# Kernel optimization log

Hardware: AMD Instinct MI355X
Metric: run time of the kernel (lower is better)

The kernel has to match this reference:

```python
import jax, jax.numpy as jnp
import numpy as np

B, R, C, A, K = 32, 13, 13, 5, 20
CELL = K + 5                      # 4 coords + objectness + 20 classes
N = R * C * A                     # 845 boxes per image
THRESH = 0.5
NMS_TH = 0.4
BIAS_VALS = [1.3221, 1.73145, 3.19275, 4.00944, 5.05587,
             8.09892, 9.47112, 4.84053, 11.2364, 10.0071]


def setup_inputs() -> dict:
    key = jax.random.key(0)
    x = jax.random.normal(key, (B, R, C, A * CELL), dtype=jnp.float32)
    bias = jnp.array(BIAS_VALS, dtype=jnp.float32)  # anchor priors (w,h interleaved)
    return {"x": x, "bias": bias}


def _nms_keep(iou, scores):
    """Greedy per-class NMS. iou: [B,N,N]; scores: [B,K,N] (already thresholded).
    Returns bool keep mask [B,K,N]. Decisions are non-differentiable, so inputs
    are stop_gradient'ed by the caller."""
    Bn = scores.shape[0]
    valid = scores > THRESH
    order = jnp.argsort(-scores, axis=-1)          # descending score order [B,K,N]
    rank = jnp.argsort(order, axis=-1)             # inverse permutation   [B,K,N]
    barange = jnp.arange(Bn)[:, None]

    def body(i, suppressed):
        idx = order[:, :, i]                                              # [B,K]
        sup_i = jnp.take_along_axis(suppressed, idx[:, :, None], -1)[..., 0]
        val_i = jnp.take_along_axis(valid, idx[:, :, None], -1)[..., 0]
        alive = val_i & ~sup_i                                            # [B,K]
        row = iou[barange, idx]                                           # [B,K,N]
        return suppressed | (alive[..., None] & (row > NMS_TH) & (rank > i))

    suppressed = jax.lax.fori_loop(0, N, body, jnp.zeros((Bn, K, N), bool))
    return valid & ~suppressed


def reference(x, bias):
    Bn, R_, C_, _ = x.shape
    t = x.reshape(Bn, R_, C_, A, CELL)
    gx = jnp.arange(C_, dtype=x.dtype)
    gy = jnp.arange(R_, dtype=x.dtype)
    # box decode (matches source: hNorm=rows used for width, wNorm=cols for height)
    bx = (jax.nn.sigmoid(t[..., 0]) + gx[None, None, :, None]) / C_
    by = (jax.nn.sigmoid(t[..., 1]) + gy[None, :, None, None]) / R_
    bw = jnp.exp(t[..., 2]) * bias[0::2] / R_
    bh = jnp.exp(t[..., 3]) * bias[1::2] / C_
    obj = jax.nn.sigmoid(t[..., 4])
    cls = jax.nn.softmax(t[..., 5:], axis=-1)
    prob = obj[..., None] * cls
    prob = jnp.where(prob > THRESH, prob, 0.0)

    # flatten to box index layout (y*cols + x)*anchors + a, same as source
    flat = lambda a: a.reshape(Bn, N)
    bx, by, bw, bh, obj = map(flat, (bx, by, bw, bh, obj))
    prob = prob.reshape(Bn, N, K)

    # corner-form boxes for IoU (source uses x - w/2, y - h/2, w, h)
    x1 = bx - bw * 0.5
    y1 = by - bh * 0.5
    x2 = x1 + bw
    y2 = y1 + bh
    iw = jnp.maximum(0.0, jnp.minimum(x2[:, :, None], x2[:, None, :]) -
                          jnp.maximum(x1[:, :, None], x1[:, None, :]))
    ih = jnp.maximum(0.0, jnp.minimum(y2[:, :, None], y2[:, None, :]) -
                          jnp.maximum(y1[:, :, None], y1[:, None, :]))
    inter = iw * ih
    area = bw * bh
    union = area[:, :, None] + area[:, None, :] - inter
    iou = inter / jnp.maximum(union, 1e-9)                       # [B,N,N]

    scores = prob.transpose(0, 2, 1)                             # [B,K,N]
    keep = _nms_keep(jax.lax.stop_gradient(iou),
                     jax.lax.stop_gradient(scores))
    out_prob = jnp.where(keep, scores, 0.0).transpose(0, 2, 1)   # [B,N,K]

    out = jnp.concatenate([bx[..., None], by[..., None], bw[..., None],
                           bh[..., None], obj[..., None], out_prob], axis=-1)
    return out  # [B, N, CELL]
```

## Files before the change

kernel.cpp:

```cpp
#include <hip/hip_runtime.h>
#include <math.h>

#define BN 32
#define RR 13
#define CC 13
#define AA 5
#define KK 20
#define CELLSZ 25
#define NN (RR * CC * AA)
#define NBK (BN * KK)
#define THRESH 0.5f
#define NMS_TH 0.4f

#define CAND_OFF 4096
#define REC 8
#define CAP NN

__device__ __forceinline__ float sigmoidf_(float x) {
    return 1.0f / (1.0f + expf(-x));
}

__global__ __launch_bounds__(256) void decode_kernel(
        const float* __restrict__ x,
        const float* __restrict__ bias,
        float* __restrict__ out,
        int* __restrict__ cnt,
        float* __restrict__ cand) {
    int idx = blockIdx.x * 256 + threadIdx.x;
    if (idx >= BN * NN) return;
    int b   = idx / NN;
    int n   = idx % NN;
    int r   = n / (CC * AA);
    int rem = n % (CC * AA);
    int c   = rem / AA;
    int a   = rem % AA;

    const float* t = x + (size_t)idx * CELLSZ;

    float bx  = (sigmoidf_(t[0]) + (float)c) / (float)CC;
    float by  = (sigmoidf_(t[1]) + (float)r) / (float)RR;
    float bw  = expf(t[2]) * bias[2 * a]     / (float)RR;
    float bh  = expf(t[3]) * bias[2 * a + 1] / (float)CC;
    float obj = sigmoidf_(t[4]);

    float l[KK];
    float m = t[5];
#pragma unroll
    for (int k = 0; k < KK; ++k) { l[k] = t[5 + k]; m = fmaxf(m, l[k]); }
    float s = 0.0f;
#pragma unroll
    for (int k = 0; k < KK; ++k) { l[k] = expf(l[k] - m); s += l[k]; }

    float* o = out + (size_t)idx * CELLSZ;
    o[0] = bx; o[1] = by; o[2] = bw; o[3] = bh; o[4] = obj;
#pragma unroll
    for (int k = 0; k < KK; ++k) o[5 + k] = 0.0f;

#pragma unroll
    for (int k = 0; k < KK; ++k) {
        float p = obj * (l[k] / s);
        if (p > THRESH) {
            int bk   = b * KK + k;
            int slot = atomicAdd(&cnt[bk], 1);
            float* rec = cand + ((size_t)bk * CAP + slot) * REC;
            float x1 = bx - bw * 0.5f;
            float y1 = by - bh * 0.5f;
            rec[0] = __int_as_float(n);
            rec[1] = p;
            rec[2] = x1;
            rec[3] = y1;
            rec[4] = x1 + bw;
            rec[5] = y1 + bh;
            rec[6] = bw * bh;
        }
    }
}

__global__ __launch_bounds__(64) void nms_kernel(
        const int* __restrict__ cnt,
        const float* __restrict__ cand,
        float* __restrict__ out) {
    int bk = blockIdx.x;
    int m  = cnt[bk];
    if (m <= 0) return;
    int b    = bk / KK;
    int k    = bk % KK;
    int lane = threadIdx.x;
    const float* list = cand + (size_t)bk * CAP * REC;

    if (m == 1) {
        if (lane == 0) {
            int n = __float_as_int(list[0]);
            out[((size_t)b * NN + n) * CELLSZ + 5 + k] = list[1];
        }
        return;
    }

    int T = (m + 63) >> 6;
    unsigned alive = 0;
    for (int tt = 0; tt < T; ++tt) {
        int j = lane + (tt << 6);
        if (j < m) alive |= 1u << tt;
    }

    while (true) {
        float bs = -1.0f;
        int   bn = 0x7fffffff;
        int   bg = -1;
        for (int tt = 0; tt < T; ++tt) {
            if ((alive >> tt) & 1u) {
                int j = lane + (tt << 6);
                float sc = list[j * REC + 1];
                int   nn = __float_as_int(list[j * REC]);
                if (sc > bs || (sc == bs && nn < bn)) { bs = sc; bn = nn; bg = j; }
            }
        }
#pragma unroll
        for (int off = 32; off > 0; off >>= 1) {
            float os = __shfl_xor(bs, off);
            int   on = __shfl_xor(bn, off);
            int   og = __shfl_xor(bg, off);
            if (os > bs || (os == bs && on < bn)) { bs = os; bn = on; bg = og; }
        }
        if (bg < 0) break;

        float X1 = list[bg * REC + 2];
        float Y1 = list[bg * REC + 3];
        float X2 = list[bg * REC + 4];
        float Y2 = list[bg * REC + 5];
        float AR = list[bg * REC + 6];

        if ((bg & 63) == lane) {
            out[((size_t)b * NN + bn) * CELLSZ + 5 + k] = bs;
            alive &= ~(1u << (bg >> 6));
        }

        for (int tt = 0; tt < T; ++tt) {
            int j = lane + (tt << 6);
            if (((alive >> tt) & 1u) && j != bg) {
                float iw = fmaxf(0.0f, fminf(X2, list[j * REC + 4]) - fmaxf(X1, list[j * REC + 2]));
                float ih = fmaxf(0.0f, fminf(Y2, list[j * REC + 5]) - fmaxf(Y1, list[j * REC + 3]));
                float inter = iw * ih;
                float uni   = AR + list[j * REC + 6] - inter;
                float iou   = inter / fmaxf(uni, 1e-9f);
                if (iou > NMS_TH) alive &= ~(1u << tt);
            }
        }
    }
}

extern "C" void kernel_launch(void* const* d_in, const int* in_sizes, int n_in,
                              void* d_out, int out_size, void* d_ws, size_t ws_size,
                              hipStream_t stream) {
    const float* x    = (const float*)d_in[0];
    const float* bias = (const float*)d_in[1];
    float* out = (float*)d_out;

    int*   cnt  = (int*)d_ws;
    float* cand = (float*)((char*)d_ws + CAND_OFF);

    hipMemsetAsync(cnt, 0, NBK * sizeof(int), stream);
    decode_kernel<<<(BN * NN + 255) / 256, 256, 0, stream>>>(x, bias, out, cnt, cand);
    nms_kernel<<<NBK, 64, 0, stream>>>(cnt, cand, out);
}
```

Measured before the change: 62.23 us.

## Fuse decode and per-class NMS into one block per image using LDS candidates

Replaces the memset, decode and NMS launches with a single kernel that runs one 1024-thread block per image. Candidates are gathered into a shared-memory pool tagged with class and box index, and each wave then runs greedy NMS for a subset of classes. This removes two launches, the global workspace traffic and the global atomics. In exchange only 32 blocks run, so most of the GPU sits idle. Each wave also rescans the whole pool for every class, and the pool caps candidates at one per box, which is safe because at most one class can exceed 0.5 after softmax.

```diff
diff --git a/kernel.cpp b/kernel.cpp
--- a/kernel.cpp
+++ b/kernel.cpp
@@ -8,142 +8,139 @@
 #define KK 20
 #define CELLSZ 25
 #define NN (RR * CC * AA)
-#define NBK (BN * KK)
 #define THRESH 0.5f
 #define NMS_TH 0.4f
 
-#define CAND_OFF 4096
-#define REC 8
-#define CAP NN
+#define BLOCK 1024
+#define NWAVE (BLOCK / 64)
+#define PCAP NN
+#define PSTR 9
 
 __device__ __forceinline__ float sigmoidf_(float x) {
     return 1.0f / (1.0f + expf(-x));
 }
 
-__global__ __launch_bounds__(256) void decode_kernel(
+__global__ __launch_bounds__(BLOCK) void fused_kernel(
         const float* __restrict__ x,
         const float* __restrict__ bias,
-        float* __restrict__ out,
-        int* __restrict__ cnt,
-        float* __restrict__ cand) {
-    int idx = blockIdx.x * 256 + threadIdx.x;
-    if (idx >= BN * NN) return;
-    int b   = idx / NN;
-    int n   = idx % NN;
-    int r   = n / (CC * AA);
-    int rem = n % (CC * AA);
-    int c   = rem / AA;
-    int a   = rem % AA;
+        float* __restrict__ out) {
+    __shared__ float pool[PCAP * PSTR];
+    __shared__ int pcnt;
 
-    const float* t = x + (size_t)idx * CELLSZ;
+    const int b   = blockIdx.x;
+    const int tid = threadIdx.x;
+    if (tid == 0) pcnt = 0;
+    __syncthreads();
 
-    float bx  = (sigmoidf_(t[0]) + (float)c) / (float)CC;
-    float by  = (sigmoidf_(t[1]) + (float)r) / (float)RR;
-    float bw  = expf(t[2]) * bias[2 * a]     / (float)RR;
-    float bh  = expf(t[3]) * bias[2 * a + 1] / (float)CC;
-    float obj = sigmoidf_(t[4]);
+    if (tid < NN) {
+        const int n   = tid;
+        const int r   = n / (CC * AA);
+        const int rem = n % (CC * AA);
+        const int c   = rem / AA;
+        const int a   = rem % AA;
 
-    float l[KK];
-    float m = t[5];
+        const float* t = x + ((size_t)b * NN + n) * CELLSZ;
+
+        float bx  = (sigmoidf_(t[0]) + (float)c) / (float)CC;
+        float by  = (sigmoidf_(t[1]) + (float)r) / (float)RR;
+        float bw  = expf(t[2]) * bias[2 * a]     / (float)RR;
+        float bh  = expf(t[3]) * bias[2 * a + 1] / (float)CC;
+        float obj = sigmoidf_(t[4]);
+
+        float l[KK];
+        float m = t[5];
 #pragma unroll
-    for (int k = 0; k < KK; ++k) { l[k] = t[5 + k]; m = fmaxf(m, l[k]); }
-    float s = 0.0f;
+        for (int k = 0; k < KK; ++k) { l[k] = t[5 + k]; m = fmaxf(m, l[k]); }
+        float s = 0.0f;
 #pragma unroll
-    for (int k = 0; k < KK; ++k) { l[k] = expf(l[k] - m); s += l[k]; }
+        for (int k = 0; k < KK; ++k) { l[k] = expf(l[k] - m); s += l[k]; }
 
-    float* o = out + (size_t)idx * CELLSZ;
-    o[0] = bx; o[1] = by; o[2] = bw; o[3] = bh; o[4] = obj;
+        float* o = out + ((size_t)b * NN + n) * CELLSZ;
+        o[0] = bx; o[1] = by; o[2] = bw; o[3] = bh; o[4] = obj;
 #pragma unroll
-    for (int k = 0; k < KK; ++k) o[5 + k] = 0.0f;
+        for (int k = 0; k < KK; ++k) o[5 + k] = 0.0f;
 
 #pragma unroll
-    for (int k = 0; k < KK; ++k) {
-        float p = obj * (l[k] / s);
-        if (p > THRESH) {
-            int bk   = b * KK + k;
-            int slot = atomicAdd(&cnt[bk], 1);
-            float* rec = cand + ((size_t)bk * CAP + slot) * REC;
-            float x1 = bx - bw * 0.5f;
-            float y1 = by - bh * 0.5f;
-            rec[0] = __int_as_float(n);
-            rec[1] = p;
-            rec[2] = x1;
-            rec[3] = y1;
-            rec[4] = x1 + bw;
-            rec[5] = y1 + bh;
-            rec[6] = bw * bh;
+        for (int k = 0; k < KK; ++k) {
+            float p = obj * (l[k] / s);
+            if (p > THRESH) {
+                int slot = atomicAdd(&pcnt, 1);
+                if (slot < PCAP) {
+                    float* rec = pool + slot * PSTR;
+                    float x1 = bx - bw * 0.5f;
+                    float y1 = by - bh * 0.5f;
+                    rec[0] = __int_as_float((k << 10) | n);
+                    rec[1] = p;
+                    rec[2] = x1;
+                    rec[3] = y1;
+                    rec[4] = x1 + bw;
+                    rec[5] = y1 + bh;
+                    rec[6] = bw * bh;
+                }
+            }
         }
     }
-}
+    __syncthreads();
 
-__global__ __launch_bounds__(64) void nms_kernel(
-        const int* __restrict__ cnt,
-        const float* __restrict__ cand,
-        float* __restrict__ out) {
-    int bk = blockIdx.x;
-    int m  = cnt[bk];
-    if (m <= 0) return;
-    int b    = bk / KK;
-    int k    = bk % KK;
-    int lane = threadIdx.x;
-    const float* list = cand + (size_t)bk * CAP * REC;
+    const int pc = min(pcnt, PCAP);
+    if (pc == 0) return;
+    const int wave = tid >> 6;
+    const int lane = tid & 63;
+    const int T = (pc + 63) >> 6;
 
-    if (m == 1) {
-        if (lane == 0) {
-            int n = __float_as_int(list[0]);
-            out[((size_t)b * NN + n) * CELLSZ + 5 + k] = list[1];
-        }
-        return;
-    }
-
-    int T = (m + 63) >> 6;
-    unsigned alive = 0;
-    for (int tt = 0; tt < T; ++tt) {
-        int j = lane + (tt << 6);
-        if (j < m) alive |= 1u << tt;
-    }
-
-    while (true) {
-        float bs = -1.0f;
-        int   bn = 0x7fffffff;
-        int   bg = -1;
+    for (int k = wave; k < KK; k += NWAVE) {
+        unsigned alive = 0;
         for (int tt = 0; tt < T; ++tt) {
-            if ((alive >> tt) & 1u) {
-                int j = lane + (tt << 6);
-                float sc = list[j * REC + 1];
-                int   nn = __float_as_int(list[j * REC]);
-                if (sc > bs || (sc == bs && nn < bn)) { bs = sc; bn = nn; bg = j; }
+            int j = lane + (tt << 6);
+            if (j < pc) {
+                int nk = __float_as_int(pool[j * PSTR]);
+                if ((nk >> 10) == k) alive |= 1u << tt;
             }
         }
+        if (__ballot(alive != 0) == 0ull) continue;
+
+        while (true) {
+            float bs = -1.0f;
+            int   bn = 0x7fffffff;
+            int   bg = -1;
+            for (int tt = 0; tt < T; ++tt) {
+                if ((alive >> tt) & 1u) {
+                    int j = lane + (tt << 6);
+                    float sc = pool[j * PSTR + 1];
+                    int   nn = __float_as_int(pool[j * PSTR]) & 1023;
+                    if (sc > bs || (sc == bs && nn < bn)) { bs = sc; bn = nn; bg = j; }
+                }
+            }
 #pragma unroll
-        for (int off = 32; off > 0; off >>= 1) {
-            float os = __shfl_xor(bs, off);
-            int   on = __shfl_xor(bn, off);
-            int   og = __shfl_xor(bg, off);
-            if (os > bs || (os == bs && on < bn)) { bs = os; bn = on; bg = og; }
-        }
-        if (bg < 0) break;
+            for (int off = 32; off > 0; off >>= 1) {
+                float os = __shfl_xor(bs, off);
+                int   on = __shfl_xor(bn, off);
+                int   og = __shfl_xor(bg, off);
+                if (os > bs || (os == bs && on < bn)) { bs = os; bn = on; bg = og; }
+            }
+            if (bg < 0) break;
 
-        float X1 = list[bg * REC + 2];
-        float Y1 = list[bg * REC + 3];
-        float X2 = list[bg * REC + 4];
-        float Y2 = list[bg * REC + 5];
-        float AR = list[bg * REC + 6];
+            float X1 = pool[bg * PSTR + 2];
+            float Y1 = pool[bg * PSTR + 3];
+            float X2 = pool[bg * PSTR + 4];
+            float Y2 = pool[bg * PSTR + 5];
+            float AR = pool[bg * PSTR + 6];
 
-        if ((bg & 63) == lane) {
-            out[((size_t)b * NN + bn) * CELLSZ + 5 + k] = bs;
-            alive &= ~(1u << (bg >> 6));
-        }
+            if ((bg & 63) == lane) {
+                out[((size_t)b * NN + bn) * CELLSZ + 5 + k] = bs;
+                alive &= ~(1u << (bg >> 6));
+            }
 
-        for (int tt = 0; tt < T; ++tt) {
-            int j = lane + (tt << 6);
-            if (((alive >> tt) & 1u) && j != bg) {
-                float iw = fmaxf(0.0f, fminf(X2, list[j * REC + 4]) - fmaxf(X1, list[j * REC + 2]));
-                float ih = fmaxf(0.0f, fminf(Y2, list[j * REC + 5]) - fmaxf(Y1, list[j * REC + 3]));
-                float inter = iw * ih;
-                float uni   = AR + list[j * REC + 6] - inter;
-                float iou   = inter / fmaxf(uni, 1e-9f);
-                if (iou > NMS_TH) alive &= ~(1u << tt);
+            for (int tt = 0; tt < T; ++tt) {
+                int j = lane + (tt << 6);
+                if (((alive >> tt) & 1u) && j != bg) {
+                    float iw = fmaxf(0.0f, fminf(X2, pool[j * PSTR + 4]) - fmaxf(X1, pool[j * PSTR + 2]));
+                    float ih = fmaxf(0.0f, fminf(Y2, pool[j * PSTR + 5]) - fmaxf(Y1, pool[j * PSTR + 3]));
+                    float inter = iw * ih;
+                    float uni   = AR + pool[j * PSTR + 6] - inter;
+                    float iou   = inter / fmaxf(uni, 1e-9f);
+                    if (iou > NMS_TH) alive &= ~(1u << tt);
+                }
             }
         }
     }
@@ -154,12 +151,5 @@
                               hipStream_t stream) {
     const float* x    = (const float*)d_in[0];
     const float* bias = (const float*)d_in[1];
-    float* out = (float*)d_out;
-
-    int*   cnt  = (int*)d_ws;
-    float* cand = (float*)((char*)d_ws + CAND_OFF);
-
-    hipMemsetAsync(cnt, 0, NBK * sizeof(int), stream);
-    decode_kernel<<<(BN * NN + 255) / 256, 256, 0, stream>>>(x, bias, out, cnt, cand);
-    nms_kernel<<<NBK, 64, 0, stream>>>(cnt, cand, out);
+    fused_kernel<<<BN, BLOCK, 0, stream>>>(x, bias, (float*)d_out);
 }
```

Result: no change. 63.25 us (+1.6%).
